# Kernel tuning notes

Measured on AMD Instinct MI355X. Metric: run time of the kernel, lower is better.

The kernel has to match this reference:

```python
import jax, jax.numpy as jnp
import numpy as np

U = 300      # lstmUnit
D = 300      # embedding dim
T = 16384    # sequence length
ADIM = 350   # attentionDimension
R = 30       # multipleAttentions


def setup_inputs() -> dict:
    key = jax.random.key(0)
    ks = jax.random.split(key, 10)
    s = 0.05
    return {
        "embedding": jax.random.normal(ks[0], (1, T, D), jnp.float32),
        # Keras LSTM packs gates as [i, f, c, o] along the last axis.
        "Wk_f": jax.random.normal(ks[1], (D, 4 * U), jnp.float32) * s,
        "Wr_f": jax.random.normal(ks[2], (U, 4 * U), jnp.float32) * s,
        "b_f": jnp.zeros((4 * U,), jnp.float32),
        "Wk_b": jax.random.normal(ks[3], (D, 4 * U), jnp.float32) * s,
        "Wr_b": jax.random.normal(ks[4], (U, 4 * U), jnp.float32) * s,
        "b_b": jnp.zeros((4 * U,), jnp.float32),
        # W1 initialized as softmax(uniform) exactly like the TF code; it's a plain variable afterwards.
        "W1": jax.nn.softmax(jax.random.uniform(ks[5], (ADIM, 2 * U), jnp.float32), axis=-1),
        "W2": jax.random.uniform(ks[6], (R, ADIM), jnp.float32),
        "dense_w": jax.random.normal(ks[7], (2 * U, 1), jnp.float32) * s,
        "dense_b": jnp.zeros((1,), jnp.float32),
    }


def _lstm(x, Wk, Wr, b, reverse):
    # x: [T, D]. Precompute input projections as one big GEMM; scan only the recurrence.
    xp = x @ Wk + b                     # [T, 4U]
    if reverse:
        xp = xp[::-1]

    def step(carry, xt):
        h, c = carry
        # activation=sigmoid on the LSTM: candidate g AND output squash use sigmoid,
        # recurrent_activation (i, f, o gates) is also sigmoid -> one fused sigmoid.
        z = jax.nn.sigmoid(xt + h @ Wr)          # [4U]
        i, f, g, o = jnp.split(z, 4)
        c = f * c + i * g
        h = o * jax.nn.sigmoid(c)
        return (h, c), h

    init = (jnp.zeros((U,), x.dtype), jnp.zeros((U,), x.dtype))
    _, hs = jax.lax.scan(step, init, xp)         # [T, U]
    if reverse:
        hs = hs[::-1]
    return hs


def reference(embedding, Wk_f, Wr_f, b_f, Wk_b, Wr_b, b_b, W1, W2, dense_w, dense_b):
    x = embedding[0]                              # squeeze batch -> [T, D]
    hf = _lstm(x, Wk_f, Wr_f, b_f, reverse=False)
    hb = _lstm(x, Wk_b, Wr_b, b_b, reverse=True)
    H = jnp.concatenate([hf, hb], axis=-1)        # [T, 2U]
    # A = softmax(W2 @ tanh(W1 @ H^T)) over the time axis (tf default axis=-1)
    A = jax.nn.softmax(W2 @ jnp.tanh(W1 @ H.T), axis=-1)   # [R, T]
    Ma = A @ H                                    # [R, 2U]
    return jax.nn.sigmoid(jnp.mean(Ma @ dense_w + dense_b))
```

## Files before the change

### kernel.cpp

```cpp
#include <hip/hip_runtime.h>
#include <cstdint>

#define TSEQ   16384
#define NCH    24
#define WARM   96

static const size_t MA_OFF    = 0;
static const size_t STATS_OFF = 18000;
static const size_t XPF_OFF   = 18064;
static const size_t XPB_OFF   = 19678864;
static const size_t H_OFF     = 39339664;
static const size_t L_OFF     = 49170064;
static const size_t HX_OFF    = 49170064;
static const size_t ST_OFF    = XPF_OFF;

__global__ __launch_bounds__(256) void gemm_xp(
    const float* __restrict__ x,
    const float* __restrict__ Wk_f, const float* __restrict__ b_f,
    const float* __restrict__ Wk_b, const float* __restrict__ b_b,
    float* __restrict__ ws)
{
    const int mt = blockIdx.x, nt = blockIdx.y, dz = blockIdx.z;
    const float* __restrict__ Wk   = dz ? Wk_b : Wk_f;
    const float* __restrict__ bias = dz ? b_b : b_f;
    float* __restrict__ out = ws + (dz ? XPB_OFF : XPF_OFF);
    const int t0 = mt * 128, n0 = nt * 128;
    __shared__ __align__(16) float As[30][129];
    __shared__ __align__(16) float Bs[30][133];
    const int tid = threadIdx.x;
    const int tx = tid & 15, ty = tid >> 4;
    float acc[8][8];
#pragma unroll
    for (int i = 0; i < 8; ++i)
#pragma unroll
        for (int j = 0; j < 8; ++j) acc[i][j] = 0.f;

    for (int k0 = 0; k0 < 300; k0 += 30) {
        for (int i = tid; i < 3840; i += 256) {
            int kk = i % 30, mm = i / 30;
            As[kk][mm] = x[(size_t)(t0 + mm) * 300 + k0 + kk];
        }
        for (int i = tid; i < 3840; i += 256) {
            int nn = i & 127, kk = i >> 7;
            int gn = n0 + nn;
            Bs[kk][nn] = (gn < 1200) ? Wk[(size_t)(k0 + kk) * 1200 + gn] : 0.f;
        }
        __syncthreads();
#pragma unroll 2
        for (int kk = 0; kk < 30; ++kk) {
            float4 a0 = *(const float4*)&As[kk][ty * 8];
            float4 a1 = *(const float4*)&As[kk][ty * 8 + 4];
            float4 b0 = *(const float4*)&Bs[kk][tx * 8];
            float4 b1 = *(const float4*)&Bs[kk][tx * 8 + 4];
            float av[8] = {a0.x, a0.y, a0.z, a0.w, a1.x, a1.y, a1.z, a1.w};
            float bv[8] = {b0.x, b0.y, b0.z, b0.w, b1.x, b1.y, b1.z, b1.w};
#pragma unroll
            for (int i = 0; i < 8; ++i)
#pragma unroll
                for (int j = 0; j < 8; ++j)
                    acc[i][j] = fmaf(av[i], bv[j], acc[i][j]);
        }
        __syncthreads();
    }
    const int gn = n0 + tx * 8;
    if (gn < 1200) {
        float4 bv0 = *(const float4*)&bias[gn];
        float4 bv1 = *(const float4*)&bias[gn + 4];
#pragma unroll
        for (int i = 0; i < 8; ++i) {
            float* orow = out + (size_t)(t0 + ty * 8 + i) * 1200 + gn;
            float4 v0 = make_float4(acc[i][0] + bv0.x, acc[i][1] + bv0.y,
                                    acc[i][2] + bv0.z, acc[i][3] + bv0.w);
            float4 v1 = make_float4(acc[i][4] + bv1.x, acc[i][5] + bv1.y,
                                    acc[i][6] + bv1.z, acc[i][7] + bv1.w);
            *(float4*)orow = v0;
            *(float4*)(orow + 4) = v1;
        }
    }
}

__device__ __forceinline__ void matvec75x2(const float* __restrict__ hl,
                                           const float (&w)[2][75],
                                           float& a0, float& a1)
{
#pragma unroll
    for (int qq = 0; qq < 18; ++qq) {
        float4 hv = *(const float4*)(hl + qq * 4);
        a0 = fmaf(hv.x, w[0][qq * 4 + 0], a0); a1 = fmaf(hv.x, w[1][qq * 4 + 0], a1);
        a0 = fmaf(hv.y, w[0][qq * 4 + 1], a0); a1 = fmaf(hv.y, w[1][qq * 4 + 1], a1);
        a0 = fmaf(hv.z, w[0][qq * 4 + 2], a0); a1 = fmaf(hv.z, w[1][qq * 4 + 2], a1);
        a0 = fmaf(hv.w, w[0][qq * 4 + 3], a0); a1 = fmaf(hv.w, w[1][qq * 4 + 3], a1);
    }
#pragma unroll
    for (int kk = 72; kk < 75; ++kk) {
        float hv = hl[kk];
        a0 = fmaf(hv, w[0][kk], a0); a1 = fmaf(hv, w[1][kk], a1);
    }
}

__global__ __launch_bounds__(512, 1) void lstm_scan(
    const float* __restrict__ Wr_f, const float* __restrict__ Wr_b,
    float* __restrict__ ws)
{
    const int tid = threadIdx.x;
    const int id = blockIdx.x;
    const int xcd = id & 7, q = id >> 3;
    const int mem = q % 5;
    const int G = xcd * 6 + q / 5;
    const int dir = G / NCH, chunk = G % NCH;
    const int u0 = mem * 60;

    const float* __restrict__ Wr = dir ? Wr_b : Wr_f;
    const float* __restrict__ xp = ws + (dir ? XPB_OFF : XPF_OFF);
    float* __restrict__ H = ws + H_OFF;
    unsigned long long* __restrict__ hx =
        (unsigned long long*)(ws + HX_OFF) + (size_t)(dir * NCH + chunk) * 2 * 304;

    const int t_begin = chunk * 682 + (chunk < 16 ? chunk : 16);
    const int S_c = 682 + (chunk < 16 ? 1 : 0);
    const int t_end = t_begin + S_c;
    int rec0, nsteps;
    if (dir == 0) {
        rec0 = t_begin - WARM; if (rec0 < 0) rec0 = 0;
        nsteps = t_end - rec0;
    } else {
        rec0 = t_end - 1 + WARM; if (rec0 > TSEQ - 1) rec0 = TSEQ - 1;
        nsteps = rec0 - t_begin + 1;
    }

    __shared__ __align__(16) float h_lds[4 * 80];
    __shared__ __align__(16) float z_lds[240];

    const int cg = tid >> 2, rr4 = tid & 3;
    float w[2][75];
    if (tid < 480) {
#pragma unroll
        for (int c = 0; c < 2; ++c) {
            int jj = 2 * cg + c;
            int gam = jj / 60;
            int gcol = gam * 300 + u0 + (jj - gam * 60);
            const float* wp = Wr + (size_t)(rr4 * 75) * 1200 + gcol;
#pragma unroll
            for (int kk = 0; kk < 75; ++kk) w[c][kk] = wp[(size_t)kk * 1200];
        }
    }
    float cstate = 0.f;
    for (int i = tid; i < 320; i += 512) h_lds[i] = 0.f;

    int pw0 = 0, pw1 = 0, pw2 = 0, pw3 = 0;
    int pp0 = 0, pp1 = 0, pp2 = 0, pp3 = 0, own_pos = 0;
    if (tid < 60) {
        int m0 = mem + 1; if (m0 >= 5) m0 -= 5;
        int m1 = mem + 2; if (m1 >= 5) m1 -= 5;
        int m2 = mem + 3; if (m2 >= 5) m2 -= 5;
        int m3 = mem + 4; if (m3 >= 5) m3 -= 5;
        pw0 = m0 * 60 + tid; pw1 = m1 * 60 + tid;
        pw2 = m2 * 60 + tid; pw3 = m3 * 60 + tid;
        pp0 = (pw0 / 75) * 80 + (pw0 % 75);
        pp1 = (pw1 / 75) * 80 + (pw1 % 75);
        pp2 = (pw2 / 75) * 80 + (pw2 % 75);
        pp3 = (pw3 / 75) * 80 + (pw3 % 75);
        int ou = u0 + tid;
        own_pos = (ou / 75) * 80 + (ou % 75);
    }

    float xq0 = 0.f, xq1 = 0.f, xq2 = 0.f, xq3 = 0.f;
    if (tid < 60) {
        const float* xr = xp + (size_t)rec0 * 1200 + u0 + tid;
        xq0 = xr[0]; xq1 = xr[300]; xq2 = xr[600]; xq3 = xr[900];
    }
    __syncthreads();

    for (int s = 0; s < nsteps; ++s) {
        const int t = (dir == 0) ? (rec0 + s) : (rec0 - s);
        const float xpv0 = xq0, xpv1 = xq1, xpv2 = xq2, xpv3 = xq3;

        if (tid < 480) {
            float a0 = 0.f, a1 = 0.f;
            matvec75x2(h_lds + rr4 * 80, w, a0, a1);
            a0 += __shfl_xor(a0, 1); a0 += __shfl_xor(a0, 2);
            a1 += __shfl_xor(a1, 1); a1 += __shfl_xor(a1, 2);
            if (rr4 == 0) { z_lds[2 * cg] = a0; z_lds[2 * cg + 1] = a1; }
        }
        __syncthreads();
        if (tid < 60) {
            float zi = xpv0 + z_lds[tid];
            float zf = xpv1 + z_lds[60 + tid];
            float zg = xpv2 + z_lds[120 + tid];
            float zo = xpv3 + z_lds[180 + tid];
            float gi = 1.f / (1.f + __expf(-zi));
            float gf = 1.f / (1.f + __expf(-zf));
            float gg = 1.f / (1.f + __expf(-zg));
            float go = 1.f / (1.f + __expf(-zo));
            cstate = gf * cstate + gi * gg;
            float h = go / (1.f + __expf(-cstate));
            unsigned long long pk =
                (((unsigned long long)(unsigned)(s + 1)) << 32) |
                (unsigned long long)__float_as_uint(h);
            __hip_atomic_store(&hx[(size_t)(s & 1) * 304 + u0 + tid], pk,
                               __ATOMIC_RELAXED, __HIP_MEMORY_SCOPE_SYSTEM);
            h_lds[own_pos] = h;
            bool emit = (dir == 0) ? (t >= t_begin) : (t < t_end);
            if (emit) H[(size_t)t * 600 + dir * 300 + u0 + tid] = h;
            if (s + 1 < nsteps) {
                const unsigned tag = (unsigned)(s + 1);
                unsigned long long* slot = hx + (size_t)(s & 1) * 304;
                unsigned long long v0 = 0, v1 = 0, v2 = 0, v3 = 0;
                bool o0 = false, o1 = false, o2 = false, o3 = false;
                int spin = 0;
                for (;;) {
                    if (!o0) v0 = __hip_atomic_load(slot + pw0, __ATOMIC_RELAXED, __HIP_MEMORY_SCOPE_SYSTEM);
                    if (!o1) v1 = __hip_atomic_load(slot + pw1, __ATOMIC_RELAXED, __HIP_MEMORY_SCOPE_SYSTEM);
                    if (!o2) v2 = __hip_atomic_load(slot + pw2, __ATOMIC_RELAXED, __HIP_MEMORY_SCOPE_SYSTEM);
                    if (!o3) v3 = __hip_atomic_load(slot + pw3, __ATOMIC_RELAXED, __HIP_MEMORY_SCOPE_SYSTEM);
                    o0 = ((unsigned)(v0 >> 32) == tag);
                    o1 = ((unsigned)(v1 >> 32) == tag);
                    o2 = ((unsigned)(v2 >> 32) == tag);
                    o3 = ((unsigned)(v3 >> 32) == tag);
                    if (o0 && o1 && o2 && o3) break;
                    if (++spin > 3) __builtin_amdgcn_s_sleep(1);
                }
                h_lds[pp0] = __uint_as_float((unsigned)v0);
                h_lds[pp1] = __uint_as_float((unsigned)v1);
                h_lds[pp2] = __uint_as_float((unsigned)v2);
                h_lds[pp3] = __uint_as_float((unsigned)v3);
                int tn = (dir == 0) ? (t + 1) : (t - 1);
                const float* xr = xp + (size_t)tn * 1200 + u0 + tid;
                xq0 = xr[0]; xq1 = xr[300]; xq2 = xr[600]; xq3 = xr[900];
            }
        }
        __syncthreads();
    }
}

__global__ __launch_bounds__(256) void gemm_st(
    const float* __restrict__ W1, float* __restrict__ ws)
{
    const int mt = blockIdx.x, nt = blockIdx.y;
    const float* __restrict__ H = ws + H_OFF;
    float* __restrict__ St = ws + ST_OFF;
    const int t0 = mt * 128, n0 = nt * 128;
    __shared__ __align__(16) float As[30][129];
    __shared__ __align__(16) float Bs[30][133];
    const int tid = threadIdx.x;
    const int tx = tid & 15, ty = tid >> 4;
    float acc[8][8];
#pragma unroll
    for (int i = 0; i < 8; ++i)
#pragma unroll
        for (int j = 0; j < 8; ++j) acc[i][j] = 0.f;

    for (int k0 = 0; k0 < 600; k0 += 30) {
        for (int i = tid; i < 3840; i += 256) {
            int kk = i % 30, mm = i / 30;
            As[kk][mm] = H[(size_t)(t0 + mm) * 600 + k0 + kk];
        }
        for (int i = tid; i < 3840; i += 256) {
            int kk = i % 30, aa = i / 30;
            int ga = n0 + aa;
            Bs[kk][aa] = (ga < 350) ? W1[(size_t)ga * 600 + k0 + kk] : 0.f;
        }
        __syncthreads();
#pragma unroll 2
        for (int kk = 0; kk < 30; ++kk) {
            float4 a0 = *(const float4*)&As[kk][ty * 8];
            float4 a1 = *(const float4*)&As[kk][ty * 8 + 4];
            float4 b0 = *(const float4*)&Bs[kk][tx * 8];
            float4 b1 = *(const float4*)&Bs[kk][tx * 8 + 4];
            float av[8] = {a0.x, a0.y, a0.z, a0.w, a1.x, a1.y, a1.z, a1.w};
            float bv[8] = {b0.x, b0.y, b0.z, b0.w, b1.x, b1.y, b1.z, b1.w};
#pragma unroll
            for (int i = 0; i < 8; ++i)
#pragma unroll
                for (int j = 0; j < 8; ++j)
                    acc[i][j] = fmaf(av[i], bv[j], acc[i][j]);
        }
        __syncthreads();
    }
    const int ga = n0 + tx * 8;
    if (ga < 352) {
#pragma unroll
        for (int i = 0; i < 8; ++i) {
            float v[8];
#pragma unroll
            for (int j = 0; j < 8; ++j)
                v[j] = 1.f - 2.f / (1.f + __expf(2.f * acc[i][j]));
            float* orow = St + (size_t)(t0 + ty * 8 + i) * 352 + ga;
            *(float4*)orow = make_float4(v[0], v[1], v[2], v[3]);
            *(float4*)(orow + 4) = make_float4(v[4], v[5], v[6], v[7]);
        }
    }
}

__global__ __launch_bounds__(256) void attn_l(
    const float* __restrict__ W2, float* __restrict__ ws)
{
    const int t0 = blockIdx.x * 64;
    const float* __restrict__ St = ws + ST_OFF;
    float* __restrict__ L = ws + L_OFF;
    __shared__ __align__(16) float Sc[64][66];
    __shared__ __align__(16) float W2c[32][66];
    const int tid = threadIdx.x;
    const int wv = tid >> 6, tt = tid & 63;
    float acc[8];
#pragma unroll
    for (int i = 0; i < 8; ++i) acc[i] = 0.f;

    for (int ac = 0; ac < 350; ac += 64) {
        __syncthreads();
        for (int i = tid; i < 4096; i += 256) {
            int aa = i & 63, t2 = i >> 6;
            int ga = ac + aa;
            Sc[aa][t2] = (ga < 350) ? St[(size_t)(t0 + t2) * 352 + ga] : 0.f;
        }
        for (int i = tid; i < 2048; i += 256) {
            int aa = i & 63, r2 = i >> 6;
            int ga = ac + aa;
            W2c[r2][aa] = (r2 < 30 && ga < 350) ? W2[(size_t)r2 * 350 + ga] : 0.f;
        }
        __syncthreads();
#pragma unroll 4
        for (int aa = 0; aa < 64; ++aa) {
            float s = Sc[aa][tt];
#pragma unroll
            for (int r8 = 0; r8 < 8; ++r8)
                acc[r8] = fmaf(W2c[wv * 8 + r8][aa], s, acc[r8]);
        }
    }
#pragma unroll
    for (int r8 = 0; r8 < 8; ++r8) {
        int r = wv * 8 + r8;
        if (r < 30) L[(size_t)r * 16384 + t0 + tt] = acc[r8];
    }
}

__global__ __launch_bounds__(256) void softmax_stats(float* __restrict__ ws)
{
    const int rrow = blockIdx.x;
    const float* __restrict__ Lr = ws + L_OFF + (size_t)rrow * 16384;
    float* __restrict__ stats = ws + STATS_OFF;
    __shared__ float red[256];
    const int tid = threadIdx.x;
    float m = -3.4e38f;
    for (int i = tid; i < 16384; i += 256) m = fmaxf(m, Lr[i]);
    red[tid] = m; __syncthreads();
    for (int s2 = 128; s2 > 0; s2 >>= 1) {
        if (tid < s2) red[tid] = fmaxf(red[tid], red[tid + s2]);
        __syncthreads();
    }
    m = red[0];
    __syncthreads();
    float sum = 0.f;
    for (int i = tid; i < 16384; i += 256) sum += __expf(Lr[i] - m);
    red[tid] = sum; __syncthreads();
    for (int s2 = 128; s2 > 0; s2 >>= 1) {
        if (tid < s2) red[tid] += red[tid + s2];
        __syncthreads();
    }
    if (tid == 0) { stats[rrow * 2] = m; stats[rrow * 2 + 1] = red[0]; }
}

__global__ __launch_bounds__(256) void ma_accum(float* __restrict__ ws)
{
    const float* __restrict__ H = ws + H_OFF;
    const float* __restrict__ L = ws + L_OFF;
    const float* __restrict__ stats = ws + STATS_OFF;
    float* __restrict__ Ma = ws + MA_OFF;
    const int t0 = blockIdx.x * 128;
    const int tid = threadIdx.x;
    __shared__ float avs[2][32];
    float accA[30], accB[30], accC[30];
#pragma unroll
    for (int r2 = 0; r2 < 30; ++r2) { accA[r2] = 0.f; accB[r2] = 0.f; accC[r2] = 0.f; }
    float mr = 0.f, isr = 0.f;
    if (tid < 30) {
        mr = stats[tid * 2]; isr = 1.f / stats[tid * 2 + 1];
        avs[0][tid] = __expf(L[(size_t)tid * 16384 + t0] - mr) * isr;
    }
    __syncthreads();
    for (int tt = 0; tt < 128; ++tt) {
        int t = t0 + tt;
        float h0 = H[(size_t)t * 600 + tid];
        float h1 = H[(size_t)t * 600 + 256 + tid];
        float h2 = (tid < 88) ? H[(size_t)t * 600 + 512 + tid] : 0.f;
        if (tt + 1 < 128 && tid < 30)
            avs[(tt + 1) & 1][tid] = __expf(L[(size_t)tid * 16384 + t + 1] - mr) * isr;
        const float* av = avs[tt & 1];
#pragma unroll
        for (int r2 = 0; r2 < 30; ++r2) {
            float a = av[r2];
            accA[r2] = fmaf(a, h0, accA[r2]);
            accB[r2] = fmaf(a, h1, accB[r2]);
            accC[r2] = fmaf(a, h2, accC[r2]);
        }
        __syncthreads();
    }
#pragma unroll
    for (int r2 = 0; r2 < 30; ++r2) {
        atomicAdd(&Ma[r2 * 600 + tid], accA[r2]);
        atomicAdd(&Ma[r2 * 600 + 256 + tid], accB[r2]);
        if (tid < 88) atomicAdd(&Ma[r2 * 600 + 512 + tid], accC[r2]);
    }
}

__global__ void final_out(const float* __restrict__ dw, const float* __restrict__ db,
                          const float* __restrict__ ws, float* __restrict__ out)
{
    const float* __restrict__ Ma = ws + MA_OFF;
    __shared__ float red[256];
    const int tid = threadIdx.x;
    float p = 0.f;
    for (int i = tid; i < 18000; i += 256) {
        int c = i % 600;
        p = fmaf(Ma[i], dw[c], p);
    }
    red[tid] = p;
    __syncthreads();
    for (int s2 = 128; s2 > 0; s2 >>= 1) {
        if (tid < s2) red[tid] += red[tid + s2];
        __syncthreads();
    }
    if (tid == 0) {
        float mval = red[0] / 30.f + db[0];
        out[0] = 1.f / (1.f + __expf(-mval));
    }
}

extern "C" void kernel_launch(void* const* d_in, const int* in_sizes, int n_in,
                              void* d_out, int out_size, void* d_ws, size_t ws_size,
                              hipStream_t stream)
{
    const float* x    = (const float*)d_in[0];
    const float* Wk_f = (const float*)d_in[1];
    const float* Wr_f = (const float*)d_in[2];
    const float* b_f  = (const float*)d_in[3];
    const float* Wk_b = (const float*)d_in[4];
    const float* Wr_b = (const float*)d_in[5];
    const float* b_b  = (const float*)d_in[6];
    const float* W1   = (const float*)d_in[7];
    const float* W2   = (const float*)d_in[8];
    const float* dw   = (const float*)d_in[9];
    const float* db   = (const float*)d_in[10];
    float* ws  = (float*)d_ws;
    float* out = (float*)d_out;

    hipMemsetAsync(d_ws, 0, 18000 * sizeof(float), stream);

    gemm_xp<<<dim3(128, 10, 2), 256, 0, stream>>>(x, Wk_f, b_f, Wk_b, b_b, ws);
    lstm_scan<<<240, 512, 0, stream>>>(Wr_f, Wr_b, ws);
    gemm_st<<<dim3(128, 3), 256, 0, stream>>>(W1, ws);
    attn_l<<<256, 256, 0, stream>>>(W2, ws);
    softmax_stats<<<30, 256, 0, stream>>>(ws);
    ma_accum<<<128, 256, 0, stream>>>(ws);
    final_out<<<1, 256, 0, stream>>>(dw, db, ws, out);
}
```

Before: 2.339 ms.

## Pack recurrent weights as bf16 pairs to fit two scan blocks per CU

Recurrent weights are stored in registers as packed bf16 pairs, with round-to-nearest-even, instead of fp32. This halves register use so the launch bound allows two 512-thread blocks per CU. The sequence is split into 48 chunks per direction instead of 24, launching 480 blocks, which halves the serial steps per chunk, and each weight column's K dimension is now split across 2 threads instead of 4. The XCD-aware block-to-group mapping is dropped, and bf16 weights lower matvec precision in the recurrence.

New measurement: 2.865 ms. +22.5%, slower.

```diff
diff --git a/kernel.cpp b/kernel.cpp
--- a/kernel.cpp
+++ b/kernel.cpp
@@ -2,7 +2,7 @@
 #include <cstdint>
 
 #define TSEQ   16384
-#define NCH    24
+#define NCHD   48
 #define WARM   96
 
 static const size_t MA_OFF    = 0;
@@ -79,45 +79,24 @@
     }
 }
 
-__device__ __forceinline__ void matvec75x2(const float* __restrict__ hl,
-                                           const float (&w)[2][75],
-                                           float& a0, float& a1)
-{
-#pragma unroll
-    for (int qq = 0; qq < 18; ++qq) {
-        float4 hv = *(const float4*)(hl + qq * 4);
-        a0 = fmaf(hv.x, w[0][qq * 4 + 0], a0); a1 = fmaf(hv.x, w[1][qq * 4 + 0], a1);
-        a0 = fmaf(hv.y, w[0][qq * 4 + 1], a0); a1 = fmaf(hv.y, w[1][qq * 4 + 1], a1);
-        a0 = fmaf(hv.z, w[0][qq * 4 + 2], a0); a1 = fmaf(hv.z, w[1][qq * 4 + 2], a1);
-        a0 = fmaf(hv.w, w[0][qq * 4 + 3], a0); a1 = fmaf(hv.w, w[1][qq * 4 + 3], a1);
-    }
-#pragma unroll
-    for (int kk = 72; kk < 75; ++kk) {
-        float hv = hl[kk];
-        a0 = fmaf(hv, w[0][kk], a0); a1 = fmaf(hv, w[1][kk], a1);
-    }
-}
-
-__global__ __launch_bounds__(512, 1) void lstm_scan(
+__global__ __launch_bounds__(512, 2) void lstm_scan(
     const float* __restrict__ Wr_f, const float* __restrict__ Wr_b,
     float* __restrict__ ws)
 {
     const int tid = threadIdx.x;
     const int id = blockIdx.x;
-    const int xcd = id & 7, q = id >> 3;
-    const int mem = q % 5;
-    const int G = xcd * 6 + q / 5;
-    const int dir = G / NCH, chunk = G % NCH;
+    const int grp = id / 5, mem = id % 5;
+    const int dir = grp / NCHD, chunk = grp % NCHD;
     const int u0 = mem * 60;
 
     const float* __restrict__ Wr = dir ? Wr_b : Wr_f;
     const float* __restrict__ xp = ws + (dir ? XPB_OFF : XPF_OFF);
     float* __restrict__ H = ws + H_OFF;
     unsigned long long* __restrict__ hx =
-        (unsigned long long*)(ws + HX_OFF) + (size_t)(dir * NCH + chunk) * 2 * 304;
-
-    const int t_begin = chunk * 682 + (chunk < 16 ? chunk : 16);
-    const int S_c = 682 + (chunk < 16 ? 1 : 0);
+        (unsigned long long*)(ws + HX_OFF) + (size_t)grp * 2 * 304;
+
+    const int t_begin = chunk * 341 + (chunk < 16 ? chunk : 16);
+    const int S_c = 341 + (chunk < 16 ? 1 : 0);
     const int t_end = t_begin + S_c;
     int rec0, nsteps;
     if (dir == 0) {
@@ -128,24 +107,26 @@
         nsteps = rec0 - t_begin + 1;
     }
 
-    __shared__ __align__(16) float h_lds[4 * 80];
+    __shared__ __align__(16) float h_lds[2 * 152];
     __shared__ __align__(16) float z_lds[240];
 
-    const int cg = tid >> 2, rr4 = tid & 3;
-    float w[2][75];
+    const int jj = tid >> 1, kh = tid & 1;
+    unsigned wp[75];
     if (tid < 480) {
-#pragma unroll
-        for (int c = 0; c < 2; ++c) {
-            int jj = 2 * cg + c;
-            int gam = jj / 60;
-            int gcol = gam * 300 + u0 + (jj - gam * 60);
-            const float* wp = Wr + (size_t)(rr4 * 75) * 1200 + gcol;
-#pragma unroll
-            for (int kk = 0; kk < 75; ++kk) w[c][kk] = wp[(size_t)kk * 1200];
+        const int gam = jj / 60;
+        const int gcol = gam * 300 + u0 + (jj - gam * 60);
+        const float* wb = Wr + (size_t)(kh * 150) * 1200 + gcol;
+#pragma unroll
+        for (int i = 0; i < 75; ++i) {
+            unsigned ua = __float_as_uint(wb[(size_t)(2 * i) * 1200]);
+            unsigned ub = __float_as_uint(wb[(size_t)(2 * i + 1) * 1200]);
+            ua = (ua + 0x7fffu + ((ua >> 16) & 1u)) >> 16;
+            ub = (ub + 0x7fffu + ((ub >> 16) & 1u)) & 0xffff0000u;
+            wp[i] = ua | ub;
         }
     }
     float cstate = 0.f;
-    for (int i = tid; i < 320; i += 512) h_lds[i] = 0.f;
+    for (int i = tid; i < 304; i += 512) h_lds[i] = 0.f;
 
     int pw0 = 0, pw1 = 0, pw2 = 0, pw3 = 0;
     int pp0 = 0, pp1 = 0, pp2 = 0, pp3 = 0, own_pos = 0;
@@ -156,12 +137,12 @@
         int m3 = mem + 4; if (m3 >= 5) m3 -= 5;
         pw0 = m0 * 60 + tid; pw1 = m1 * 60 + tid;
         pw2 = m2 * 60 + tid; pw3 = m3 * 60 + tid;
-        pp0 = (pw0 / 75) * 80 + (pw0 % 75);
-        pp1 = (pw1 / 75) * 80 + (pw1 % 75);
-        pp2 = (pw2 / 75) * 80 + (pw2 % 75);
-        pp3 = (pw3 / 75) * 80 + (pw3 % 75);
+        pp0 = (pw0 / 150) * 152 + (pw0 % 150);
+        pp1 = (pw1 / 150) * 152 + (pw1 % 150);
+        pp2 = (pw2 / 150) * 152 + (pw2 % 150);
+        pp3 = (pw3 / 150) * 152 + (pw3 % 150);
         int ou = u0 + tid;
-        own_pos = (ou / 75) * 80 + (ou % 75);
+        own_pos = (ou / 150) * 152 + (ou % 150);
     }
 
     float xq0 = 0.f, xq1 = 0.f, xq2 = 0.f, xq3 = 0.f;
@@ -176,11 +157,24 @@
         const float xpv0 = xq0, xpv1 = xq1, xpv2 = xq2, xpv3 = xq3;
 
         if (tid < 480) {
-            float a0 = 0.f, a1 = 0.f;
-            matvec75x2(h_lds + rr4 * 80, w, a0, a1);
-            a0 += __shfl_xor(a0, 1); a0 += __shfl_xor(a0, 2);
-            a1 += __shfl_xor(a1, 1); a1 += __shfl_xor(a1, 2);
-            if (rr4 == 0) { z_lds[2 * cg] = a0; z_lds[2 * cg + 1] = a1; }
+            const float* hl = h_lds + kh * 152;
+            float a = 0.f;
+#pragma unroll
+            for (int i = 0; i < 37; ++i) {
+                float4 hv = *(const float4*)(hl + 4 * i);
+                unsigned ua = wp[2 * i], ub = wp[2 * i + 1];
+                a = fmaf(hv.x, __uint_as_float(ua << 16), a);
+                a = fmaf(hv.y, __uint_as_float(ua & 0xffff0000u), a);
+                a = fmaf(hv.z, __uint_as_float(ub << 16), a);
+                a = fmaf(hv.w, __uint_as_float(ub & 0xffff0000u), a);
+            }
+            {
+                unsigned uc = wp[74];
+                a = fmaf(hl[148], __uint_as_float(uc << 16), a);
+                a = fmaf(hl[149], __uint_as_float(uc & 0xffff0000u), a);
+            }
+            a += __shfl_xor(a, 1);
+            if (kh == 0) z_lds[jj] = a;
         }
         __syncthreads();
         if (tid < 60) {
@@ -447,7 +441,7 @@
     hipMemsetAsync(d_ws, 0, 18000 * sizeof(float), stream);
 
     gemm_xp<<<dim3(128, 10, 2), 256, 0, stream>>>(x, Wk_f, b_f, Wk_b, b_b, ws);
-    lstm_scan<<<240, 512, 0, stream>>>(Wr_f, Wr_b, ws);
+    lstm_scan<<<480, 512, 0, stream>>>(Wr_f, Wr_b, ws);
     gemm_st<<<dim3(128, 3), 256, 0, stream>>>(W1, ws);
     attn_l<<<256, 256, 0, stream>>>(W2, ws);
     softmax_stats<<<30, 256, 0, stream>>>(ws);
```
